# Kernel optimization log

Hardware: AMD Instinct MI355X
Metric: run time of the kernel (lower is better)

## Reference

```python
import jax, jax.numpy as jnp
import numpy as np

N_NODES = 50000
N_EDGES = 800000
N_GRAPHS = 64
IN_DIM = 768
HID = 256
OUT_DIM = 4
N_REL = 3
N_LAYERS = 3


def setup_inputs() -> dict:
    key = jax.random.key(0)
    ks = jax.random.split(key, 20)
    inp = {
        "x": jax.random.normal(ks[0], (N_NODES, IN_DIM), dtype=jnp.float32),
        "edge_index": jax.random.randint(ks[1], (2, N_EDGES), 0, N_NODES, dtype=jnp.int32),
        "edge_type": jax.random.randint(ks[2], (N_EDGES,), 0, N_REL, dtype=jnp.int32),
        "batch": jnp.sort(jax.random.randint(ks[3], (N_NODES,), 0, N_GRAPHS, dtype=jnp.int32)),
        # input projection
        "in_w": jax.random.normal(ks[4], (IN_DIM, HID), dtype=jnp.float32) * (IN_DIM ** -0.5),
        "in_b": jnp.zeros((HID,), dtype=jnp.float32),
        # RGCN layers (stacked over num_layers)
        "root_w": jax.random.normal(ks[5], (N_LAYERS, HID, HID), dtype=jnp.float32) * (HID ** -0.5),
        "rel_w": jax.random.normal(ks[6], (N_LAYERS, N_REL, HID, HID), dtype=jnp.float32) * (HID ** -0.5),
        "conv_b": jnp.zeros((N_LAYERS, HID), dtype=jnp.float32),
        "ln_w": jnp.ones((N_LAYERS, HID), dtype=jnp.float32),
        "ln_b": jnp.zeros((N_LAYERS, HID), dtype=jnp.float32),
        # classifier MLP
        "cls_w1": jax.random.normal(ks[7], (HID, HID), dtype=jnp.float32) * (HID ** -0.5),
        "cls_b1": jnp.zeros((HID,), dtype=jnp.float32),
        "cls_w2": jax.random.normal(ks[8], (HID, OUT_DIM), dtype=jnp.float32) * (HID ** -0.5),
        "cls_b2": jnp.zeros((OUT_DIM,), dtype=jnp.float32),
    }
    return inp


def _rgcn_conv(h, src, dst, edge_type, root, rel, bias):
    # PyG RGCNConv (default aggr='mean'): out = h @ root + sum_r mean_dst(h[src] | type==r) @ W_r + b
    n = h.shape[0]
    out = h @ root + bias
    for r in range(N_REL):
        m = (edge_type == r).astype(h.dtype)  # [E]
        msg = h[src] * m[:, None]             # gather + mask
        s = jax.ops.segment_sum(msg, dst, num_segments=n)   # [N, HID]
        cnt = jax.ops.segment_sum(m, dst, num_segments=n)   # [N]
        mean = s / jnp.maximum(cnt, 1.0)[:, None]
        out = out + mean @ rel[r]
    return out


def _layer_norm(h, w, b, eps=1e-5):
    mu = jnp.mean(h, axis=-1, keepdims=True)
    var = jnp.mean((h - mu) ** 2, axis=-1, keepdims=True)
    return (h - mu) * jax.lax.rsqrt(var + eps) * w + b


def reference(x, edge_index, edge_type, batch, in_w, in_b, root_w, rel_w, conv_b,
              ln_w, ln_b, cls_w1, cls_b1, cls_w2, cls_b2):
    src, dst = edge_index[0], edge_index[1]
    h = x @ in_w + in_b
    for i in range(N_LAYERS):
        h_new = _rgcn_conv(h, src, dst, edge_type, root_w[i], rel_w[i], conv_b[i])
        h = h_new + h  # residual (shapes always equal: HID->HID)
        h = jax.nn.relu(h)
        h = _layer_norm(h, ln_w[i], ln_b[i])
        # dropout is identity in eval mode
    # global max pool over each graph
    g = jax.ops.segment_max(h, batch, num_segments=N_GRAPHS)  # [B, HID]
    z = jax.nn.relu(g @ cls_w1 + cls_b1)
    return z @ cls_w2 + cls_b2
```

## Files before the change

kernel.cpp:

```cpp
#include <hip/hip_runtime.h>
#include <cstdint>
#include <cstddef>

#define NN 50000
#define NE 800000
#define NG 64
#define IND 768
#define HID 256
#define NREL 3
#define NLAY 3

typedef __attribute__((ext_vector_type(4))) float f32x4;
typedef __attribute__((ext_vector_type(8))) short s16x8;
typedef __attribute__((ext_vector_type(4))) unsigned short u16x4;

__global__ void k_zero_int(int* __restrict__ p, int n) {
  int i = blockIdx.x * 256 + threadIdx.x;
  if (i < n) p[i] = 0;
}

__global__ void k_hist(const int* __restrict__ dst, int* __restrict__ deg) {
  int e = blockIdx.x * 256 + threadIdx.x;
  if (e < NE) atomicAdd(&deg[dst[e]], 1);
}

__global__ __launch_bounds__(1024) void k_scan(const int* __restrict__ deg,
                                               int* __restrict__ row_start,
                                               int* __restrict__ cursor) {
  __shared__ int wsum[16];
  int t = threadIdx.x;
  int lane = t & 63, wid = t >> 6;
  int running = 0;
  if (t == 0) row_start[0] = 0;
  for (int base = 0; base < NN; base += 4096) {
    int idx = base + t * 4;
    int4 d = *(const int4*)(deg + idx);
    int s = d.x + d.y + d.z + d.w;
    int sc = s;
    #pragma unroll
    for (int off = 1; off < 64; off <<= 1) {
      int o = __shfl_up(sc, off);
      if (lane >= off) sc += o;
    }
    if (lane == 63) wsum[wid] = sc;
    __syncthreads();
    if (t == 0) {
      int a = 0;
      #pragma unroll
      for (int i = 0; i < 16; ++i) { a += wsum[i]; wsum[i] = a; }
    }
    __syncthreads();
    int woff = (wid == 0) ? 0 : wsum[wid - 1];
    int excl = running + woff + (sc - s);
    int e0 = excl, e1 = e0 + d.x, e2 = e1 + d.y, e3 = e2 + d.z, e4 = e3 + d.w;
    if (idx     < NN) { cursor[idx]     = e0; row_start[idx + 1] = e1; }
    if (idx + 1 < NN) { cursor[idx + 1] = e1; row_start[idx + 2] = e2; }
    if (idx + 2 < NN) { cursor[idx + 2] = e2; row_start[idx + 3] = e3; }
    if (idx + 3 < NN) { cursor[idx + 3] = e3; row_start[idx + 4] = e4; }
    running += wsum[15];
    __syncthreads();
  }
}

__global__ void k_scatter(const int* __restrict__ src, const int* __restrict__ dst,
                          const int* __restrict__ ety, int* __restrict__ cursor,
                          unsigned* __restrict__ csr) {
  int e = blockIdx.x * 256 + threadIdx.x;
  if (e >= NE) return;
  int pos = atomicAdd(&cursor[dst[e]], 1);
  csr[pos] = (unsigned)src[e] | ((unsigned)ety[e] << 16);
}

__global__ void k_graph_bounds(const int* __restrict__ batch, int* __restrict__ gstart) {
  int i = blockIdx.x * 256 + threadIdx.x;
  if (i >= NN) return;
  int b = batch[i];
  int bp = (i == 0) ? -1 : batch[i - 1];
  for (int g = bp + 1; g <= b; ++g) gstart[g] = i;
  if (i == NN - 1) {
    for (int g = b + 1; g <= NG; ++g) gstart[g] = NN;
  }
}

__device__ __forceinline__ unsigned short bf16rne(float f) {
  union { float f; unsigned u; } x; x.f = f;
  unsigned r = (x.u + 0x7FFFu + ((x.u >> 16) & 1u)) >> 16;
  return (unsigned short)r;
}
__device__ __forceinline__ float bf2f(unsigned short h) {
  union { unsigned u; float f; } x; x.u = ((unsigned)h) << 16;
  return x.f;
}

__global__ __launch_bounds__(64) void k_aggregate(const float* __restrict__ h,
                                                  const int* __restrict__ row_start,
                                                  const unsigned* __restrict__ csr,
                                                  unsigned short* __restrict__ aggH,
                                                  unsigned short* __restrict__ aggL) {
  int n = blockIdx.x;
  int t = threadIdx.x;
  int s = row_start[n], e = row_start[n + 1];
  float4 a0 = {0, 0, 0, 0}, a1 = {0, 0, 0, 0}, a2 = {0, 0, 0, 0};
  int c0 = 0, c1 = 0, c2 = 0;
  __shared__ unsigned buf[64];
  for (int base = s; base < e; base += 64) {
    int m = e - base; if (m > 64) m = 64;
    __syncthreads();
    if (t < m) buf[t] = csr[base + t];
    __syncthreads();
    for (int j = 0; j < m; ++j) {
      unsigned p = buf[j];
      int src = p & 0xFFFF;
      int ty = (int)(p >> 16);
      float4 v = *(const float4*)(h + (size_t)src * HID + t * 4);
      if (ty == 0)      { a0.x += v.x; a0.y += v.y; a0.z += v.z; a0.w += v.w; c0++; }
      else if (ty == 1) { a1.x += v.x; a1.y += v.y; a1.z += v.z; a1.w += v.w; c1++; }
      else              { a2.x += v.x; a2.y += v.y; a2.z += v.z; a2.w += v.w; c2++; }
    }
  }
  float i0 = 1.f / (float)(c0 > 1 ? c0 : 1);
  float i1 = 1.f / (float)(c1 > 1 ? c1 : 1);
  float i2 = 1.f / (float)(c2 > 1 ? c2 : 1);
  float vr[12] = {a0.x * i0, a0.y * i0, a0.z * i0, a0.w * i0,
                  a1.x * i1, a1.y * i1, a1.z * i1, a1.w * i1,
                  a2.x * i2, a2.y * i2, a2.z * i2, a2.w * i2};
  size_t ob = (size_t)n * (NREL * HID) + t * 4;
  #pragma unroll
  for (int r = 0; r < 3; ++r) {
    u16x4 hv, lv;
    #pragma unroll
    for (int j = 0; j < 4; ++j) {
      unsigned short hh = bf16rne(vr[r * 4 + j]);
      hv[j] = hh;
      lv[j] = bf16rne(vr[r * 4 + j] - bf2f(hh));
    }
    *(u16x4*)(aggH + ob + r * HID) = hv;
    *(u16x4*)(aggL + ob + r * HID) = lv;
  }
}

__global__ void k_cvt(const float* __restrict__ s1, int K1e,
                      const float* __restrict__ s2, int Ktot,
                      unsigned short* __restrict__ hi, unsigned short* __restrict__ lo) {
  int t = blockIdx.x * 256 + threadIdx.x;
  if (t >= Ktot * 256) return;
  int c = t & 255, k = t >> 8;
  float v = (k < K1e) ? s1[(size_t)k * 256 + c] : s2[(size_t)(k - K1e) * 256 + c];
  unsigned short h = bf16rne(v);
  unsigned short l = bf16rne(v - bf2f(h));
  size_t o = ((size_t)(k >> 3) * 256 + c) * 8 + (k & 7);
  hi[o] = h; lo[o] = l;
}

__device__ __forceinline__ void load_lds16b(const void* g, void* l) {
  __builtin_amdgcn_global_load_lds(
      (const __attribute__((address_space(1))) unsigned*)g,
      (__attribute__((address_space(3))) unsigned*)l, 16, 0, 0);
}

__global__ __launch_bounds__(256, 1) void k_gemm_in(
    const float* __restrict__ A1,
    const unsigned short* __restrict__ Bhi, const unsigned short* __restrict__ Blo,
    const float* __restrict__ bias,
    float* __restrict__ C, unsigned short* __restrict__ Ch, unsigned short* __restrict__ Cl,
    int M) {
  const int K = IND;
  __shared__ __align__(16) unsigned short AsH[4 * 64 * 8], AsL[4 * 64 * 8];
  __shared__ __align__(16) unsigned short BsH[4 * 256 * 8], BsL[4 * 256 * 8];
  int tid = (int)threadIdx.x;
  int lane = tid & 63, wv = tid >> 6;
  int n0 = (int)blockIdx.x * 64;
  int srow = tid >> 2, sg = tid & 3;
  int grow = n0 + srow; if (grow > M - 1) grow = M - 1;
  int c16 = lane & 15, kg = lane >> 4;
  int col0 = wv * 64;

  f32x4 acc[4][4] = {};
  int nkt = K / 32;

  float4 a0, a1;
  {
    const float* ap = A1 + (size_t)grow * IND + sg * 8;
    a0 = *(const float4*)ap;
    a1 = *(const float4*)(ap + 4);
  }

  for (int kt = 0; kt < nkt; ++kt) {
    __syncthreads();
    #pragma unroll
    for (int i = 0; i < 8; ++i) {
      int id = wv * 8 + i;
      const unsigned short* srcp = (id < 16) ? Bhi : Blo;
      unsigned short* dstp = (id < 16) ? BsH : BsL;
      int rem = id & 15, g = rem >> 2, ch = rem & 3;
      load_lds16b(srcp + (size_t)(kt * 4 + g) * 2048 + (ch * 64 + lane) * 8,
                  dstp + (g * 256 + ch * 64) * 8);
    }
    {
      float va[8] = {a0.x, a0.y, a0.z, a0.w, a1.x, a1.y, a1.z, a1.w};
      s16x8 hv, lv;
      #pragma unroll
      for (int j = 0; j < 8; ++j) {
        unsigned short h = bf16rne(va[j]);
        hv[j] = (short)h;
        lv[j] = (short)bf16rne(va[j] - bf2f(h));
      }
      int aoff = (sg * 64 + (srow ^ (sg << 2))) * 8;
      *(s16x8*)&AsH[aoff] = hv;
      *(s16x8*)&AsL[aoff] = lv;
    }
    __syncthreads();
    s16x8 ah[4], al[4];
    #pragma unroll
    for (int ri = 0; ri < 4; ++ri) {
      int ao = (kg * 64 + ((ri * 16 + c16) ^ (kg << 2))) * 8;
      ah[ri] = *(const s16x8*)&AsH[ao];
      al[ri] = *(const s16x8*)&AsL[ao];
    }
    int kn = (kt + 1) * 32;
    if (kn < K) {
      const float* ap = A1 + (size_t)grow * IND + kn + sg * 8;
      a0 = *(const float4*)ap;
      a1 = *(const float4*)(ap + 4);
    }
    #pragma unroll
    for (int ci = 0; ci < 4; ++ci) {
      int bo = (kg * 256 + col0 + ci * 16 + c16) * 8;
      s16x8 bh = *(const s16x8*)&BsH[bo];
      s16x8 bl = *(const s16x8*)&BsL[bo];
      #pragma unroll
      for (int ri = 0; ri < 4; ++ri) {
        acc[ri][ci] = __builtin_amdgcn_mfma_f32_16x16x32_bf16(ah[ri], bh, acc[ri][ci], 0, 0, 0);
        acc[ri][ci] = __builtin_amdgcn_mfma_f32_16x16x32_bf16(ah[ri], bl, acc[ri][ci], 0, 0, 0);
        acc[ri][ci] = __builtin_amdgcn_mfma_f32_16x16x32_bf16(al[ri], bh, acc[ri][ci], 0, 0, 0);
      }
    }
  }

  float bw[4];
  #pragma unroll
  for (int ci = 0; ci < 4; ++ci) bw[ci] = bias[col0 + ci * 16 + c16];
  #pragma unroll
  for (int ri = 0; ri < 4; ++ri)
    #pragma unroll
    for (int q = 0; q < 4; ++q) {
      int row = n0 + ri * 16 + kg * 4 + q;
      if (row < M) {
        #pragma unroll
        for (int ci = 0; ci < 4; ++ci) {
          float v = acc[ri][ci][q] + bw[ci];
          size_t o = (size_t)row * 256 + col0 + ci * 16 + c16;
          C[o] = v;
          unsigned short hh = bf16rne(v);
          Ch[o] = hh;
          Cl[o] = bf16rne(v - bf2f(hh));
        }
      }
    }
}

__global__ __launch_bounds__(256, 1) void k_gemm_L(
    const unsigned short* __restrict__ Ah1, const unsigned short* __restrict__ Al1,
    const unsigned short* __restrict__ Ah2, const unsigned short* __restrict__ Al2,
    const unsigned short* __restrict__ Bhi, const unsigned short* __restrict__ Blo,
    const float* __restrict__ bias, const float* __restrict__ res,
    const float* __restrict__ lnw, const float* __restrict__ lnb,
    float* __restrict__ C, unsigned short* __restrict__ Ch, unsigned short* __restrict__ Cl,
    int M) {
  const int K1 = HID, K = HID + NREL * HID;
  __shared__ __align__(16) unsigned short BsH[2][4 * 256 * 8];
  __shared__ __align__(16) unsigned short BsL[2][4 * 256 * 8];
  __shared__ float lnred[64 * 4 * 2];
  int tid = (int)threadIdx.x;
  int lane = tid & 63, wv = tid >> 6;
  int n0 = (int)blockIdx.x * 64;
  int c16 = lane & 15, kg = lane >> 4;
  int col0 = wv * 64;
  int arow[4];
  #pragma unroll
  for (int ri = 0; ri < 4; ++ri) {
    int r = n0 + ri * 16 + c16;
    arow[ri] = r < M ? r : M - 1;
  }

  f32x4 acc[4][4] = {};

  auto dmaB = [&](int kt, int b) {
    #pragma unroll
    for (int i = 0; i < 8; ++i) {
      int id = wv * 8 + i;
      const unsigned short* srcp = (id < 16) ? Bhi : Blo;
      unsigned short* dstp = (id < 16) ? &BsH[b][0] : &BsL[b][0];
      int rem = id & 15, g = rem >> 2, ch = rem & 3;
      load_lds16b(srcp + (size_t)(kt * 4 + g) * 2048 + (ch * 64 + lane) * 8,
                  dstp + (g * 256 + ch * 64) * 8);
    }
  };
  s16x8 ah[4], al[4], ahn[4] = {}, aln[4] = {};
  auto loadA = [&](int kt, s16x8* AH, s16x8* AL) {
    int kk = kt * 32;
    const unsigned short *ph, *pl; int ld, kc;
    if (kk < K1) { ph = Ah1; pl = Al1; ld = HID; kc = kk; }
    else         { ph = Ah2; pl = Al2; ld = NREL * HID; kc = kk - K1; }
    #pragma unroll
    for (int ri = 0; ri < 4; ++ri) {
      size_t o = (size_t)arow[ri] * ld + kc + kg * 8;
      AH[ri] = *(const s16x8*)(ph + o);
      AL[ri] = *(const s16x8*)(pl + o);
    }
  };

  dmaB(0, 0);
  loadA(0, ah, al);
  int cur = 0;
  const int nkt = K / 32;
  for (int kt = 0; kt < nkt; ++kt) {
    __syncthreads();
    if (kt + 1 < nkt) {
      dmaB(kt + 1, cur ^ 1);
      loadA(kt + 1, ahn, aln);
    }
    #pragma unroll
    for (int ci = 0; ci < 4; ++ci) {
      int bo = (kg * 256 + col0 + ci * 16 + c16) * 8;
      s16x8 bh = *(const s16x8*)&BsH[cur][bo];
      s16x8 bl = *(const s16x8*)&BsL[cur][bo];
      #pragma unroll
      for (int ri = 0; ri < 4; ++ri) {
        acc[ri][ci] = __builtin_amdgcn_mfma_f32_16x16x32_bf16(ah[ri], bh, acc[ri][ci], 0, 0, 0);
        acc[ri][ci] = __builtin_amdgcn_mfma_f32_16x16x32_bf16(ah[ri], bl, acc[ri][ci], 0, 0, 0);
        acc[ri][ci] = __builtin_amdgcn_mfma_f32_16x16x32_bf16(al[ri], bh, acc[ri][ci], 0, 0, 0);
      }
    }
    #pragma unroll
    for (int ri = 0; ri < 4; ++ri) { ah[ri] = ahn[ri]; al[ri] = aln[ri]; }
    cur ^= 1;
  }

  float bw[4], lw[4], lb[4];
  #pragma unroll
  for (int ci = 0; ci < 4; ++ci) {
    int col = col0 + ci * 16 + c16;
    bw[ci] = bias[col];
    lw[ci] = lnw[col];
    lb[ci] = lnb[col];
  }
  #pragma unroll
  for (int ri = 0; ri < 4; ++ri)
    #pragma unroll
    for (int q = 0; q < 4; ++q) {
      int rl = ri * 16 + kg * 4 + q;
      int rr = n0 + rl; int rc = rr < M ? rr : M - 1;
      float s = 0.f, s2 = 0.f;
      #pragma unroll
      for (int ci = 0; ci < 4; ++ci) {
        float r = res[(size_t)rc * 256 + col0 + ci * 16 + c16];
        float v = fmaxf(acc[ri][ci][q] + bw[ci] + r, 0.f);
        acc[ri][ci][q] = v;
        s += v; s2 += v * v;
      }
      #pragma unroll
      for (int m = 1; m < 16; m <<= 1) {
        s  += __shfl_xor(s, m);
        s2 += __shfl_xor(s2, m);
      }
      if (c16 == 0) {
        lnred[(rl * 4 + wv) * 2]     = s;
        lnred[(rl * 4 + wv) * 2 + 1] = s2;
      }
    }
  __syncthreads();
  #pragma unroll
  for (int ri = 0; ri < 4; ++ri)
    #pragma unroll
    for (int q = 0; q < 4; ++q) {
      int rl = ri * 16 + kg * 4 + q;
      float S = 0.f, S2 = 0.f;
      #pragma unroll
      for (int w = 0; w < 4; ++w) {
        S  += lnred[(rl * 4 + w) * 2];
        S2 += lnred[(rl * 4 + w) * 2 + 1];
      }
      float mean = S * (1.f / 256.f);
      float var = S2 * (1.f / 256.f) - mean * mean;
      float rstd = rsqrtf(var + 1e-5f);
      int row = n0 + rl;
      if (row < M) {
        #pragma unroll
        for (int ci = 0; ci < 4; ++ci) {
          float v = (acc[ri][ci][q] - mean) * rstd * lw[ci] + lb[ci];
          size_t o = (size_t)row * 256 + col0 + ci * 16 + c16;
          C[o] = v;
          unsigned short hh = bf16rne(v);
          Ch[o] = hh;
          Cl[o] = bf16rne(v - bf2f(hh));
        }
      }
    }
}

__global__ __launch_bounds__(256) void k_pool1(const float* __restrict__ h,
                                               const int* __restrict__ gstart,
                                               float* __restrict__ part) {
  int gi = blockIdx.x, ck = blockIdx.y;
  int c = (int)threadIdx.x;
  int s = gstart[gi], e = gstart[gi + 1], len = e - s;
  int cs = s + (int)(((long long)len * ck) >> 3);
  int ce = s + (int)(((long long)len * (ck + 1)) >> 3);
  float m = -3.402823466e+38f;
  int n = cs;
  for (; n + 2 <= ce; n += 2) {
    float x0 = h[(size_t)n * HID + c];
    float x1 = h[(size_t)(n + 1) * HID + c];
    m = fmaxf(m, fmaxf(x0, x1));
  }
  if (n < ce) m = fmaxf(m, h[(size_t)n * HID + c]);
  part[((size_t)gi * 8 + ck) * HID + c] = m;
}

__global__ __launch_bounds__(256) void k_pool2(const float* __restrict__ part,
                                               float* __restrict__ g) {
  int gi = blockIdx.x, c = (int)threadIdx.x;
  float m = part[((size_t)gi * 8) * HID + c];
  #pragma unroll
  for (int k = 1; k < 8; ++k) m = fmaxf(m, part[((size_t)gi * 8 + k) * HID + c]);
  g[gi * HID + c] = m;
}

__global__ __launch_bounds__(256) void k_classifier(const float* __restrict__ g,
                                                    const float* __restrict__ w1,
                                                    const float* __restrict__ b1,
                                                    const float* __restrict__ w2,
                                                    const float* __restrict__ b2,
                                                    float* __restrict__ out) {
  int gi = blockIdx.x, t = (int)threadIdx.x;
  __shared__ float gs[HID], zs[HID];
  gs[t] = g[gi * HID + t];
  __syncthreads();
  float s = b1[t];
  for (int k = 0; k < HID; ++k) s = fmaf(gs[k], w1[k * HID + t], s);
  zs[t] = fmaxf(s, 0.f);
  __syncthreads();
  if (t < 4) {
    float o = b2[t];
    for (int k = 0; k < HID; ++k) o = fmaf(zs[k], w2[k * 4 + t], o);
    out[gi * 4 + t] = o;
  }
}

extern "C" void kernel_launch(void* const* d_in, const int* in_sizes, int n_in,
                              void* d_out, int out_size, void* d_ws, size_t ws_size,
                              hipStream_t stream) {
  const float* x      = (const float*)d_in[0];
  const int*   eidx   = (const int*)d_in[1];
  const int*   etype  = (const int*)d_in[2];
  const int*   batch  = (const int*)d_in[3];
  const float* in_w   = (const float*)d_in[4];
  const float* in_b   = (const float*)d_in[5];
  const float* root_w = (const float*)d_in[6];
  const float* rel_w  = (const float*)d_in[7];
  const float* conv_b = (const float*)d_in[8];
  const float* ln_w   = (const float*)d_in[9];
  const float* ln_b   = (const float*)d_in[10];
  const float* cls_w1 = (const float*)d_in[11];
  const float* cls_b1 = (const float*)d_in[12];
  const float* cls_w2 = (const float*)d_in[13];
  const float* cls_b2 = (const float*)d_in[14];
  float* out = (float*)d_out;

  char* ws = (char*)d_ws;
  size_t off = 0;
  auto alloc = [&](size_t bytes) -> void* {
    void* p = ws + off;
    off += (bytes + 255) & ~(size_t)255;
    return p;
  };
  float*    bufA   = (float*)alloc(sizeof(float) * (size_t)NN * HID);
  float*    bufB   = (float*)alloc(sizeof(float) * (size_t)NN * HID);
  unsigned short* hAh = (unsigned short*)alloc(sizeof(unsigned short) * (size_t)NN * HID);
  unsigned short* hAl = (unsigned short*)alloc(sizeof(unsigned short) * (size_t)NN * HID);
  unsigned short* hBh = (unsigned short*)alloc(sizeof(unsigned short) * (size_t)NN * HID);
  unsigned short* hBl = (unsigned short*)alloc(sizeof(unsigned short) * (size_t)NN * HID);
  unsigned short* aggH = (unsigned short*)alloc(sizeof(unsigned short) * (size_t)NN * NREL * HID);
  unsigned short* aggL = (unsigned short*)alloc(sizeof(unsigned short) * (size_t)NN * NREL * HID);
  unsigned* csr       = (unsigned*)alloc(sizeof(unsigned) * NE);
  int*      deg       = (int*)alloc(sizeof(int) * 53248);
  int*      row_start = (int*)alloc(sizeof(int) * (NN + 1));
  int*      cursor    = (int*)alloc(sizeof(int) * NN);
  int*      gstart    = (int*)alloc(sizeof(int) * (NG + 1));
  float*    gpool     = (float*)alloc(sizeof(float) * NG * HID);
  float*    gpart     = (float*)alloc(sizeof(float) * NG * 8 * HID);
  unsigned short* wInH = (unsigned short*)alloc(sizeof(unsigned short) * 96 * 256 * 8);
  unsigned short* wInL = (unsigned short*)alloc(sizeof(unsigned short) * 96 * 256 * 8);
  unsigned short* wLH[NLAY];
  unsigned short* wLL[NLAY];
  for (int L = 0; L < NLAY; ++L) {
    wLH[L] = (unsigned short*)alloc(sizeof(unsigned short) * 128 * 256 * 8);
    wLL[L] = (unsigned short*)alloc(sizeof(unsigned short) * 128 * 256 * 8);
  }
  (void)ws_size; (void)in_sizes; (void)n_in; (void)out_size;

  const int* esrc = eidx;
  const int* edst = eidx + NE;

  k_cvt<<<IND, 256, 0, stream>>>(in_w, IND, nullptr, IND, wInH, wInL);
  for (int L = 0; L < NLAY; ++L)
    k_cvt<<<HID + NREL * HID, 256, 0, stream>>>(
        root_w + (size_t)L * HID * HID, HID,
        rel_w + (size_t)L * NREL * HID * HID, HID + NREL * HID, wLH[L], wLL[L]);

  k_zero_int<<<(53248 + 255) / 256, 256, 0, stream>>>(deg, 53248);
  k_hist<<<(NE + 255) / 256, 256, 0, stream>>>(edst, deg);
  k_scan<<<1, 1024, 0, stream>>>(deg, row_start, cursor);
  k_scatter<<<(NE + 255) / 256, 256, 0, stream>>>(esrc, edst, etype, cursor, csr);
  k_graph_bounds<<<(NN + 255) / 256, 256, 0, stream>>>(batch, gstart);

  int gemm_grid = (NN + 63) / 64;
  k_gemm_in<<<gemm_grid, 256, 0, stream>>>(x, wInH, wInL, in_b, bufA, hAh, hAl, NN);

  float* hcur = bufA;  unsigned short* hch = hAh;  unsigned short* hcl = hAl;
  float* hnxt = bufB;  unsigned short* hnh = hBh;  unsigned short* hnl = hBl;
  for (int L = 0; L < NLAY; ++L) {
    k_aggregate<<<NN, 64, 0, stream>>>(hcur, row_start, csr, aggH, aggL);
    k_gemm_L<<<gemm_grid, 256, 0, stream>>>(
        hch, hcl, aggH, aggL, wLH[L], wLL[L],
        conv_b + L * HID, hcur, ln_w + L * HID, ln_b + L * HID,
        hnxt, hnh, hnl, NN);
    float* tf = hcur; hcur = hnxt; hnxt = tf;
    unsigned short* th = hch; hch = hnh; hnh = th;
    unsigned short* tl = hcl; hcl = hnl; hnl = tl;
  }

  k_pool1<<<dim3(NG, 8), 256, 0, stream>>>(hcur, gstart, gpart);
  k_pool2<<<NG, 256, 0, stream>>>(gpart, gpool);
  k_classifier<<<NG, 256, 0, stream>>>(gpool, cls_w1, cls_b1, cls_w2, cls_b2, out);
}
```

Measured before the change: 1.463 ms.

## Stage A tiles in LDS via DMA and drop double buffering in layer GEMM

In the fused RGCN layer GEMM, the A operand (hi/lo bf16 rows) is now loaded into shared memory with direct-to-LDS loads, so the 64 rows are fetched once per block. Before, each of the four waves read the same rows from global memory into registers. To make room, the double-buffered B tiles and the register prefetch of A are replaced by a single buffer, with two barriers per k-step. The layer-norm reduction scratch now reuses the A buffer. The change saves redundant global traffic and shared memory, which may allow more blocks per CU. In exchange, loads no longer overlap the MFMA work within a block.

```diff
diff --git a/kernel.cpp b/kernel.cpp
--- a/kernel.cpp
+++ b/kernel.cpp
@@ -268,63 +268,56 @@
     float* __restrict__ C, unsigned short* __restrict__ Ch, unsigned short* __restrict__ Cl,
     int M) {
   const int K1 = HID, K = HID + NREL * HID;
-  __shared__ __align__(16) unsigned short BsH[2][4 * 256 * 8];
-  __shared__ __align__(16) unsigned short BsL[2][4 * 256 * 8];
-  __shared__ float lnred[64 * 4 * 2];
+  __shared__ __align__(16) unsigned short AsH[4 * 64 * 8], AsL[4 * 64 * 8];
+  __shared__ __align__(16) unsigned short BsH[4 * 256 * 8], BsL[4 * 256 * 8];
   int tid = (int)threadIdx.x;
   int lane = tid & 63, wv = tid >> 6;
   int n0 = (int)blockIdx.x * 64;
   int c16 = lane & 15, kg = lane >> 4;
   int col0 = wv * 64;
-  int arow[4];
-  #pragma unroll
-  for (int ri = 0; ri < 4; ++ri) {
-    int r = n0 + ri * 16 + c16;
-    arow[ri] = r < M ? r : M - 1;
-  }
+  int alane = n0 + lane; if (alane > M - 1) alane = M - 1;
 
   f32x4 acc[4][4] = {};
-
-  auto dmaB = [&](int kt, int b) {
+  const int nkt = K / 32;
+
+  for (int kt = 0; kt < nkt; ++kt) {
+    int kk = kt * 32;
+    __syncthreads();
     #pragma unroll
     for (int i = 0; i < 8; ++i) {
       int id = wv * 8 + i;
       const unsigned short* srcp = (id < 16) ? Bhi : Blo;
-      unsigned short* dstp = (id < 16) ? &BsH[b][0] : &BsL[b][0];
+      unsigned short* dstp = (id < 16) ? BsH : BsL;
       int rem = id & 15, g = rem >> 2, ch = rem & 3;
       load_lds16b(srcp + (size_t)(kt * 4 + g) * 2048 + (ch * 64 + lane) * 8,
                   dstp + (g * 256 + ch * 64) * 8);
     }
-  };
-  s16x8 ah[4], al[4], ahn[4] = {}, aln[4] = {};
-  auto loadA = [&](int kt, s16x8* AH, s16x8* AL) {
-    int kk = kt * 32;
-    const unsigned short *ph, *pl; int ld, kc;
-    if (kk < K1) { ph = Ah1; pl = Al1; ld = HID; kc = kk; }
-    else         { ph = Ah2; pl = Al2; ld = NREL * HID; kc = kk - K1; }
+    {
+      const unsigned short *ph, *pl; int ld, kc;
+      if (kk < K1) { ph = Ah1; pl = Al1; ld = HID; kc = kk; }
+      else         { ph = Ah2; pl = Al2; ld = NREL * HID; kc = kk - K1; }
+      #pragma unroll
+      for (int i = 0; i < 2; ++i) {
+        int id = wv * 2 + i;
+        int g = id & 3;
+        const unsigned short* srcp = (id < 4) ? ph : pl;
+        unsigned short* dstp = (id < 4) ? AsH : AsL;
+        load_lds16b(srcp + (size_t)alane * ld + kc + g * 8, dstp + g * 64 * 8);
+      }
+    }
+    __syncthreads();
+    s16x8 ah[4], al[4];
     #pragma unroll
     for (int ri = 0; ri < 4; ++ri) {
-      size_t o = (size_t)arow[ri] * ld + kc + kg * 8;
-      AH[ri] = *(const s16x8*)(ph + o);
-      AL[ri] = *(const s16x8*)(pl + o);
-    }
-  };
-
-  dmaB(0, 0);
-  loadA(0, ah, al);
-  int cur = 0;
-  const int nkt = K / 32;
-  for (int kt = 0; kt < nkt; ++kt) {
-    __syncthreads();
-    if (kt + 1 < nkt) {
-      dmaB(kt + 1, cur ^ 1);
-      loadA(kt + 1, ahn, aln);
+      int ao = (kg * 64 + ri * 16 + c16) * 8;
+      ah[ri] = *(const s16x8*)&AsH[ao];
+      al[ri] = *(const s16x8*)&AsL[ao];
     }
     #pragma unroll
     for (int ci = 0; ci < 4; ++ci) {
       int bo = (kg * 256 + col0 + ci * 16 + c16) * 8;
-      s16x8 bh = *(const s16x8*)&BsH[cur][bo];
-      s16x8 bl = *(const s16x8*)&BsL[cur][bo];
+      s16x8 bh = *(const s16x8*)&BsH[bo];
+      s16x8 bl = *(const s16x8*)&BsL[bo];
       #pragma unroll
       for (int ri = 0; ri < 4; ++ri) {
         acc[ri][ci] = __builtin_amdgcn_mfma_f32_16x16x32_bf16(ah[ri], bh, acc[ri][ci], 0, 0, 0);
@@ -332,11 +325,10 @@
         acc[ri][ci] = __builtin_amdgcn_mfma_f32_16x16x32_bf16(al[ri], bh, acc[ri][ci], 0, 0, 0);
       }
     }
-    #pragma unroll
-    for (int ri = 0; ri < 4; ++ri) { ah[ri] = ahn[ri]; al[ri] = aln[ri]; }
-    cur ^= 1;
-  }
-
+  }
+
+  __syncthreads();
+  float* lnred = (float*)AsH;
   float bw[4], lw[4], lb[4];
   #pragma unroll
   for (int ci = 0; ci < 4; ++ci) {
```

New measurement: 1.301 ms. 11.1% less time.
